# Optimization experiments

Measured on AMD Instinct MI355X. Metric: run time of the kernel, lower is better.

## Reference

```python
import jax, jax.numpy as jnp
import numpy as np

HID, NH, HD, MD = 512, 8, 64, 16  # hidden_dim, num_heads, head_dim, manifold_dim
B, S = 4, 1024
FLOW_STEPS, DT = 10, 0.1
EPS = 1e-8


def _cplx_weight(k, shape, std=0.02):
    kr, ki = jax.random.split(k)
    w = jax.random.normal(kr, shape) + 1j * jax.random.normal(ki, shape)
    return (w * std).astype(jnp.complex64)


def setup_inputs() -> dict:
    key = jax.random.key(0)
    ks = jax.random.split(key, 12)
    inp = {}
    inp['x_real'] = jax.random.normal(ks[0], (B, S, HID), dtype=jnp.float32)
    inp['x_imag'] = jax.random.normal(ks[1], (B, S, HID), dtype=jnp.float32)
    # manifold projection head_dim -> manifold_dim
    inp['Wm'] = _cplx_weight(ks[2], (MD, HD), std=HD ** -0.5)
    inp['bm'] = jnp.zeros((MD,), jnp.complex64)
    inp['Wq'] = _cplx_weight(ks[3], (MD, MD))
    inp['bq'] = jnp.zeros((MD,), jnp.complex64)
    inp['Wk'] = _cplx_weight(ks[4], (MD, MD))
    inp['bk'] = jnp.zeros((MD,), jnp.complex64)
    inp['Wv'] = _cplx_weight(ks[5], (MD, MD))
    inp['bv'] = jnp.zeros((MD,), jnp.complex64)
    # learned manifold metric (initialized to identity as in the module)
    inp['metric'] = jnp.eye(MD, dtype=jnp.complex64)
    # output projection expanded_dim = NH*MD -> hidden_dim
    inp['Wo'] = _cplx_weight(ks[6], (HID, NH * MD))
    inp['bo'] = jnp.zeros((HID,), jnp.complex64)
    return inp


def _forward(x_real, x_imag, Wm, bm, Wq, bq, Wk, bk, Wv, bv, metric, Wo, bo):
    x = (x_real + 1j * x_imag).astype(jnp.complex64)            # [B,S,HID]
    b, s, _ = x.shape
    h = x.reshape(b, s, NH, HD).transpose(0, 2, 1, 3)           # [B,NH,S,HD]
    # project onto low-dim manifold coordinates
    m = h @ Wm.T + bm                                           # [B,NH,S,MD]
    # hyperbolic exponential map at origin (curvature -1): tanh(|v|)/|v| * v
    n = jnp.sqrt(jnp.sum(jnp.abs(m) ** 2, -1, keepdims=True)) + EPS
    m = (jnp.tanh(n) / n) * m
    # parallel transport via the learned metric
    m = m @ metric
    # geometric flow: 10 Euler integration steps with dt=0.1
    sym = 0.5 * (metric + metric.conj().T)

    def step(carry, _):
        vel = carry @ sym - carry
        return carry + DT * vel, None

    m, _ = jax.lax.scan(step, m, None, length=FLOW_STEPS)
    # hyperbolic logarithm map at origin: artanh(|u|)/|u| * u
    n2 = jnp.sqrt(jnp.sum(jnp.abs(m) ** 2, -1, keepdims=True))
    n2 = jnp.clip(n2, EPS, 1.0 - 1e-6)
    m = (jnp.arctanh(n2) / n2) * m
    # complex q/k/v attention on manifold coordinates
    q = m @ Wq.T + bq
    k = m @ Wk.T + bk
    v = m @ Wv.T + bv
    scale = HD ** -0.5  # module uses self.scale = head_dim ** -0.5
    scores = jnp.einsum('bhsd,bhtd->bhst', q, jnp.conj(k)).real * scale  # [B,NH,S,S]
    attn = jax.nn.softmax(scores, axis=-1).astype(jnp.complex64)
    out = jnp.einsum('bhst,bhtd->bhsd', attn, v)                # [B,NH,S,MD]
    expanded = out.transpose(0, 2, 1, 3).reshape(b, s, NH * MD)  # [B,S,NH*MD]
    return expanded @ Wo.T + bo + x                              # residual, [B,S,HID]


def reference(x_real, x_imag, Wm, bm, Wq, bq, Wk, bk, Wv, bv, metric, Wo, bo):
    return _forward(x_real, x_imag, Wm, bm, Wq, bq, Wk, bk, Wv, bv, metric, Wo, bo)
```

## Files before the change

kernel.cpp:

```cpp
#include <hip/hip_runtime.h>
#include <math.h>

#define HIDD 512
#define NHH 8
#define HDD 64
#define MDD 16
#define Bz 4
#define Sz 1024
#define DTf 0.1f
#define EPSf 1e-8f
#define SCALEf 0.125f

typedef unsigned short ushort_t;
typedef unsigned int uint_t;

typedef __attribute__((ext_vector_type(8))) short bf16x8;
typedef __attribute__((ext_vector_type(4))) float f32x4;

constexpr size_t OFF_QB   = 0;
constexpr size_t OFF_KB   = OFF_QB + 262144;
constexpr size_t OFF_VT   = OFF_KB + 262144;
constexpr size_t OFF_E    = OFF_VT + 262144;
constexpr size_t OFF_T    = OFF_E + (size_t)Bz * Sz * NHH * MDD;
constexpr size_t OFF_WOT  = OFF_T + 256;
constexpr size_t OFF_FLAG = OFF_WOT + 512 * 128;

__device__ __forceinline__ float bf2f(ushort_t u) {
  union { unsigned int i; float f; } c;
  c.i = ((unsigned int)u) << 16;
  return c.f;
}
__device__ __forceinline__ ushort_t f2bf(float f) {
  unsigned int x = __float_as_uint(f);
  unsigned int r = (x + 0x7fffu + ((x >> 16) & 1u)) >> 16;
  return (ushort_t)r;
}
__device__ __forceinline__ float2 ldc(const void* p, int i, bool bf) {
  if (bf) {
    ushort2 u = ((const ushort2*)p)[i];
    return make_float2(bf2f(u.x), bf2f(u.y));
  }
  return ((const float2*)p)[i];
}
__device__ __forceinline__ float ldr(const void* p, size_t i, bool bf) {
  if (bf) return bf2f(((const ushort_t*)p)[i]);
  return ((const float*)p)[i];
}
__device__ __forceinline__ float2 cmadd(float2 acc, float2 a, float2 b) {
  acc.x = fmaf(a.x, b.x, fmaf(-a.y, b.y, acc.x));
  acc.y = fmaf(a.x, b.y, fmaf(a.y, b.x, acc.y));
  return acc;
}

__global__ __launch_bounds__(256) void k_setup(const void* __restrict__ metric,
                                               const ushort_t* __restrict__ xr_u,
                                               const void* __restrict__ Wo,
                                               int* __restrict__ flags,
                                               float2* __restrict__ Tg,
                                               float2* __restrict__ WoT) {
  __shared__ float2 mets[256], Ms[256], Ps2[256];
  __shared__ int votes[4];
  const uint_t* mu = (const uint_t*)metric;
  bool cbf = (mu[0] == 0x00003F80u);
  int tid = threadIdx.x;
  if (blockIdx.x == 0) {
    unsigned e = (xr_u[tid] >> 7) & 0xFFu;
    unsigned long long bal = __ballot(e >= 100u && e <= 134u);
    if ((tid & 63) == 0) votes[tid >> 6] = (int)__popcll(bal);
    __syncthreads();
    if (tid == 0) {
      int c = votes[0] + votes[1] + votes[2] + votes[3];
      flags[0] = cbf ? 1 : 0;
      flags[1] = (c > 192) ? 1 : 0;
    }
    int i = tid >> 4, j = tid & 15;
    mets[tid] = ldc(metric, tid, cbf);
    __syncthreads();
    float2 a = mets[tid];
    float2 bt = mets[j * 16 + i];
    float2 symv = make_float2(0.5f * (a.x + bt.x), 0.5f * (a.y - bt.y));
    float2 Mv = make_float2(DTf * symv.x, DTf * symv.y);
    if (i == j) Mv.x += 1.0f - DTf;
    Ms[tid] = Mv;
    Ps2[tid] = Mv;
    __syncthreads();
    for (int it = 0; it < 9; it++) {
      float2 acc = make_float2(0.f, 0.f);
      #pragma unroll
      for (int k = 0; k < 16; k++) acc = cmadd(acc, Ps2[i * 16 + k], Ms[k * 16 + j]);
      __syncthreads();
      Ps2[tid] = acc;
      __syncthreads();
    }
    float2 acc = make_float2(0.f, 0.f);
    #pragma unroll
    for (int k = 0; k < 16; k++) acc = cmadd(acc, mets[i * 16 + k], Ps2[k * 16 + j]);
    Tg[tid] = acc;
  } else {
    int idx = (blockIdx.x - 1) * 256 + tid;
    int o = idx >> 7, j = idx & 127;
    WoT[(size_t)j * 512 + o] = ldc(Wo, idx, cbf);
  }
}

__global__ __launch_bounds__(256) void k_qkv(
    const void* __restrict__ xr, const void* __restrict__ xi,
    const void* __restrict__ Wm, const void* __restrict__ bm,
    const void* __restrict__ Wq, const void* __restrict__ bq,
    const void* __restrict__ Wk, const void* __restrict__ bk,
    const void* __restrict__ Wv, const void* __restrict__ bv,
    const float2* __restrict__ Tg, const int* __restrict__ flags,
    ushort_t* __restrict__ Qb, ushort_t* __restrict__ Kb,
    ushort_t* __restrict__ VTb) {
  __shared__ float2 hs[64 * 65];
  __shared__ float2 msc[64 * 17];
  __shared__ float2 wmt[64 * 16];
  __shared__ float2 Tm[256];
  __shared__ float2 wqt[256], wkt[256], wvt[256];
  __shared__ float2 bms[16], bqs[16], bks[16], bvs[16];
  float2* msc2 = hs;

  bool cbf = flags[0] != 0;
  bool xbf = flags[1] != 0;
  int tid = threadIdx.x;
  int bh = blockIdx.y;
  int s0 = blockIdx.x * 64;

  size_t xoff = ((size_t)(((bh >> 3) * Sz) + s0)) * HIDD + (bh & 7) * HDD;
  if (xbf) {
    const ushort_t* xrb = (const ushort_t*)xr + xoff;
    const ushort_t* xib = (const ushort_t*)xi + xoff;
    #pragma unroll
    for (int it = 0; it < 4; it++) {
      int idx = tid + it * 256;
      int i = idx >> 4, e4 = idx & 15;
      ushort4 ur = ((const ushort4*)(xrb + (size_t)i * HIDD))[e4];
      ushort4 ui = ((const ushort4*)(xib + (size_t)i * HIDD))[e4];
      int e = e4 * 4;
      hs[i * 65 + e + 0] = make_float2(bf2f(ur.x), bf2f(ui.x));
      hs[i * 65 + e + 1] = make_float2(bf2f(ur.y), bf2f(ui.y));
      hs[i * 65 + e + 2] = make_float2(bf2f(ur.z), bf2f(ui.z));
      hs[i * 65 + e + 3] = make_float2(bf2f(ur.w), bf2f(ui.w));
    }
  } else {
    const float* xrb = (const float*)xr + xoff;
    const float* xib = (const float*)xi + xoff;
    #pragma unroll
    for (int it = 0; it < 4; it++) {
      int idx = tid + it * 256;
      int i = idx >> 4, e4 = idx & 15;
      float4 fr = ((const float4*)(xrb + (size_t)i * HIDD))[e4];
      float4 fi = ((const float4*)(xib + (size_t)i * HIDD))[e4];
      int e = e4 * 4;
      hs[i * 65 + e + 0] = make_float2(fr.x, fi.x);
      hs[i * 65 + e + 1] = make_float2(fr.y, fi.y);
      hs[i * 65 + e + 2] = make_float2(fr.z, fi.z);
      hs[i * 65 + e + 3] = make_float2(fr.w, fi.w);
    }
  }
  #pragma unroll
  for (int it = 0; it < 4; it++) {
    int c = tid + it * 256;
    int d = c >> 6, e = c & 63;
    wmt[e * 16 + d] = ldc(Wm, c, cbf);
  }
  {
    int j = tid >> 4, d = tid & 15;
    Tm[tid] = Tg[tid];
    wqt[d * 16 + j] = ldc(Wq, tid, cbf);
    wkt[d * 16 + j] = ldc(Wk, tid, cbf);
    wvt[d * 16 + j] = ldc(Wv, tid, cbf);
    if (tid < 16) {
      bms[tid] = ldc(bm, tid, cbf); bqs[tid] = ldc(bq, tid, cbf);
      bks[tid] = ldc(bk, tid, cbf); bvs[tid] = ldc(bv, tid, cbf);
    }
  }
  __syncthreads();

  int tok = tid >> 2, g = tid & 3;
  int jb = g * 4;

  float2 acc[4];
  #pragma unroll
  for (int i2 = 0; i2 < 4; i2++) acc[i2] = bms[jb + i2];
  for (int e = 0; e < 64; e++) {
    float2 hv = hs[tok * 65 + e];
    #pragma unroll
    for (int i2 = 0; i2 < 4; i2++) acc[i2] = cmadd(acc[i2], hv, wmt[e * 16 + jb + i2]);
  }
  float nn = 0.f;
  #pragma unroll
  for (int i2 = 0; i2 < 4; i2++) nn += acc[i2].x * acc[i2].x + acc[i2].y * acc[i2].y;
  nn += __shfl_xor(nn, 1);
  nn += __shfl_xor(nn, 2);
  float n1 = sqrtf(nn) + EPSf;
  float sc1 = tanhf(n1) / n1;
  #pragma unroll
  for (int i2 = 0; i2 < 4; i2++)
    msc[tok * 17 + jb + i2] = make_float2(acc[i2].x * sc1, acc[i2].y * sc1);
  __syncthreads();

  float2 m2[4];
  #pragma unroll
  for (int i2 = 0; i2 < 4; i2++) m2[i2] = make_float2(0.f, 0.f);
  for (int d = 0; d < 16; d++) {
    float2 mv = msc[tok * 17 + d];
    #pragma unroll
    for (int i2 = 0; i2 < 4; i2++) m2[i2] = cmadd(m2[i2], mv, Tm[d * 16 + jb + i2]);
  }
  float nn2 = 0.f;
  #pragma unroll
  for (int i2 = 0; i2 < 4; i2++) nn2 += m2[i2].x * m2[i2].x + m2[i2].y * m2[i2].y;
  nn2 += __shfl_xor(nn2, 1);
  nn2 += __shfl_xor(nn2, 2);
  float n2 = sqrtf(nn2);
  n2 = fminf(fmaxf(n2, EPSf), 1.0f - 1e-6f);
  float fac = atanhf(n2) / n2;
  #pragma unroll
  for (int i2 = 0; i2 < 4; i2++)
    msc2[tok * 17 + jb + i2] = make_float2(m2[i2].x * fac, m2[i2].y * fac);
  __syncthreads();

  float2 qa[4], ka[4], va[4];
  #pragma unroll
  for (int i2 = 0; i2 < 4; i2++) { qa[i2] = bqs[jb + i2]; ka[i2] = bks[jb + i2]; va[i2] = bvs[jb + i2]; }
  for (int d = 0; d < 16; d++) {
    float2 mv = msc2[tok * 17 + d];
    #pragma unroll
    for (int i2 = 0; i2 < 4; i2++) {
      qa[i2] = cmadd(qa[i2], mv, wqt[d * 16 + jb + i2]);
      ka[i2] = cmadd(ka[i2], mv, wkt[d * 16 + jb + i2]);
      va[i2] = cmadd(va[i2], mv, wvt[d * 16 + jb + i2]);
    }
  }
  int s = s0 + tok;
  uint_t qp[4], kp[4];
  #pragma unroll
  for (int i2 = 0; i2 < 4; i2++) {
    qp[i2] = (uint_t)f2bf(qa[i2].x * SCALEf) | ((uint_t)f2bf(qa[i2].y * SCALEf) << 16);
    kp[i2] = (uint_t)f2bf(ka[i2].x) | ((uint_t)f2bf(ka[i2].y) << 16);
  }
  size_t rowbase = ((size_t)bh * Sz + s) * 32 + (size_t)g * 8;
  *(uint4*)(Qb + rowbase) = make_uint4(qp[0], qp[1], qp[2], qp[3]);
  *(uint4*)(Kb + rowbase) = make_uint4(kp[0], kp[1], kp[2], kp[3]);
  size_t vtb = (size_t)bh * 32 * Sz;
  #pragma unroll
  for (int i2 = 0; i2 < 4; i2++) {
    int d = (jb + i2) * 2;
    VTb[vtb + (size_t)d * Sz + s]       = f2bf(va[i2].x);
    VTb[vtb + (size_t)(d + 1) * Sz + s] = f2bf(va[i2].y);
  }
}

__global__ __launch_bounds__(256) void k_attn_mf(const ushort_t* __restrict__ Qb,
                                                 const ushort_t* __restrict__ Kb,
                                                 const ushort_t* __restrict__ VTb,
                                                 float* __restrict__ ef) {
  __shared__ ushort_t Ks[128 * 88];
  __shared__ ushort_t VTs[32 * 152];
  __shared__ ushort_t Ps[4 * 16 * 40];
  int tid = threadIdx.x;
  int w = tid >> 6, lane = tid & 63;
  int n = lane & 15, qd = lane >> 4;
  int bh = blockIdx.y;
  int qb = blockIdx.x * 64 + w * 16;

  const ushort_t* Qh = Qb + (size_t)bh * Sz * 32;
  const ushort_t* Kh = Kb + (size_t)bh * Sz * 32;
  const ushort_t* VTh = VTb + (size_t)bh * 32 * Sz;

  bf16x8 qf = *(const bf16x8*)(Qh + (size_t)(qb + n) * 32 + qd * 8);

  f32x4 o0 = {0.f, 0.f, 0.f, 0.f}, o1 = {0.f, 0.f, 0.f, 0.f};
  float m_run = -INFINITY, l_run = 0.f;
  ushort_t* Pw = Ps + w * 16 * 40;

  for (int kc = 0; kc < Sz; kc += 128) {
    __syncthreads();
    {
      int row = tid >> 1, half = tid & 1;
      const uint4* sk = (const uint4*)(Kh + (size_t)(kc + row) * 32 + half * 16);
      uint4 a = sk[0], b2 = sk[1];
      *(uint4*)(Ks + row * 88 + half * 16) = a;
      *(uint4*)(Ks + row * 88 + half * 16 + 8) = b2;
      int d = tid >> 3, seg = tid & 7;
      const uint4* sv = (const uint4*)(VTh + (size_t)d * Sz + kc + seg * 16);
      uint4 c = sv[0], e2 = sv[1];
      *(uint4*)(VTs + d * 152 + seg * 16) = c;
      *(uint4*)(VTs + d * 152 + seg * 16 + 8) = e2;
    }
    __syncthreads();
    #pragma unroll
    for (int st = 0; st < 4; st++) {
      int kb = st * 32;
      bf16x8 ka0 = *(const bf16x8*)(Ks + (kb + n) * 88 + qd * 8);
      bf16x8 ka1 = *(const bf16x8*)(Ks + (kb + 16 + n) * 88 + qd * 8);
      f32x4 z = {0.f, 0.f, 0.f, 0.f};
      f32x4 st0 = __builtin_amdgcn_mfma_f32_16x16x32_bf16(ka0, qf, z, 0, 0, 0);
      f32x4 st1 = __builtin_amdgcn_mfma_f32_16x16x32_bf16(ka1, qf, z, 0, 0, 0);
      float mt = fmaxf(fmaxf(fmaxf(st0[0], st0[1]), fmaxf(st0[2], st0[3])),
                       fmaxf(fmaxf(st1[0], st1[1]), fmaxf(st1[2], st1[3])));
      mt = fmaxf(mt, __shfl_xor(mt, 16));
      mt = fmaxf(mt, __shfl_xor(mt, 32));
      float mnew = fmaxf(m_run, mt);
      float alpha = __expf(m_run - mnew);
      float p0[4], p1[4];
      #pragma unroll
      for (int r = 0; r < 4; r++) {
        p0[r] = __expf(st0[r] - mnew);
        p1[r] = __expf(st1[r] - mnew);
      }
      float ls = (p0[0] + p0[1]) + (p0[2] + p0[3])
               + (p1[0] + p1[1]) + (p1[2] + p1[3]);
      ls += __shfl_xor(ls, 16);
      ls += __shfl_xor(ls, 32);
      l_run = fmaf(l_run, alpha, ls);
      m_run = mnew;
      #pragma unroll
      for (int r = 0; r < 4; r++) {
        Pw[n * 40 + qd * 4 + r]      = f2bf(p0[r]);
        Pw[n * 40 + 16 + qd * 4 + r] = f2bf(p1[r]);
      }
      bf16x8 pa = *(const bf16x8*)(Pw + n * 40 + qd * 8);
      bf16x8 vb0 = *(const bf16x8*)(VTs + n * 152 + kb + qd * 8);
      bf16x8 vb1 = *(const bf16x8*)(VTs + (n + 16) * 152 + kb + qd * 8);
      float ar0 = __shfl(alpha, qd * 4 + 0);
      float ar1 = __shfl(alpha, qd * 4 + 1);
      float ar2 = __shfl(alpha, qd * 4 + 2);
      float ar3 = __shfl(alpha, qd * 4 + 3);
      f32x4 oo0, oo1;
      oo0[0] = o0[0] * ar0; oo0[1] = o0[1] * ar1; oo0[2] = o0[2] * ar2; oo0[3] = o0[3] * ar3;
      oo1[0] = o1[0] * ar0; oo1[1] = o1[1] * ar1; oo1[2] = o1[2] * ar2; oo1[3] = o1[3] * ar3;
      o0 = __builtin_amdgcn_mfma_f32_16x16x32_bf16(pa, vb0, oo0, 0, 0, 0);
      o1 = __builtin_amdgcn_mfma_f32_16x16x32_bf16(pa, vb1, oo1, 0, 0, 0);
    }
  }
  int b = bh >> 3, h = bh & 7;
  #pragma unroll
  for (int r = 0; r < 4; r++) {
    float li = __shfl(l_run, qd * 4 + r);
    float inv = 1.0f / li;
    int tok = qb + qd * 4 + r;
    float* ep = ef + (((size_t)(b * Sz + tok)) * NHH + h) * 32;
    ep[n]      = o0[r] * inv;
    ep[16 + n] = o1[r] * inv;
  }
}

__global__ __launch_bounds__(256) void k_proj_r(const float2* __restrict__ ew,
                                                const float2* __restrict__ WoT,
                                                const void* __restrict__ bo,
                                                const void* __restrict__ xr,
                                                const int* __restrict__ flags,
                                                float* __restrict__ out) {
  __shared__ float2 es[8 * 128];
  bool cbf = flags[0] != 0;
  bool xbf = flags[1] != 0;
  int tid = threadIdx.x;
  int tok0 = (blockIdx.x >> 1) * 8;
  int o = (blockIdx.x & 1) * 256 + tid;
  #pragma unroll
  for (int it = 0; it < 4; it++) {
    int idx = tid + it * 256;
    es[idx] = ew[(size_t)tok0 * 128 + idx];
  }
  __syncthreads();
  float acc[8];
  #pragma unroll
  for (int t = 0; t < 8; t++) acc[t] = 0.f;
  #pragma unroll 8
  for (int j = 0; j < 128; j++) {
    float2 w = WoT[(size_t)j * 512 + o];
    #pragma unroll
    for (int t = 0; t < 8; t++) {
      float2 e = es[t * 128 + j];
      acc[t] = fmaf(e.x, w.x, fmaf(-e.y, w.y, acc[t]));
    }
  }
  float bor = ldc(bo, o, cbf).x;
  #pragma unroll
  for (int t = 0; t < 8; t++) {
    size_t gt = tok0 + t;
    out[gt * HIDD + o] = acc[t] + bor + ldr(xr, gt * HIDD + o, xbf);
  }
}

__global__ __launch_bounds__(256) void k_proj_c(const float2* __restrict__ ew,
                                                const float2* __restrict__ WoT,
                                                const void* __restrict__ bo,
                                                const void* __restrict__ xr,
                                                const void* __restrict__ xi,
                                                const int* __restrict__ flags,
                                                ushort2* __restrict__ out) {
  __shared__ float2 es[8 * 128];
  bool cbf = flags[0] != 0;
  bool xbf = flags[1] != 0;
  int tid = threadIdx.x;
  int tok0 = blockIdx.x * 8;
  #pragma unroll
  for (int it = 0; it < 4; it++) {
    int idx = tid + it * 256;
    es[idx] = ew[(size_t)tok0 * 128 + idx];
  }
  __syncthreads();
  for (int rep = 0; rep < 2; rep++) {
    int o = tid + rep * 256;
    float2 accT[8];
    #pragma unroll
    for (int t = 0; t < 8; t++) accT[t] = make_float2(0.f, 0.f);
    #pragma unroll 2
    for (int j = 0; j < 128; j++) {
      float2 wv = WoT[(size_t)j * 512 + o];
      #pragma unroll
      for (int t = 0; t < 8; t++) accT[t] = cmadd(accT[t], es[t * 128 + j], wv);
    }
    float2 bov = ldc(bo, o, cbf);
    #pragma unroll
    for (int t = 0; t < 8; t++) {
      size_t gt = tok0 + t;
      float rx = accT[t].x + bov.x + ldr(xr, gt * HIDD + o, xbf);
      float ry = accT[t].y + bov.y + ldr(xi, gt * HIDD + o, xbf);
      out[gt * HIDD + o] = make_ushort2(f2bf(ry), f2bf(rx));
    }
  }
}

extern "C" void kernel_launch(void* const* d_in, const int* in_sizes, int n_in,
                              void* d_out, int out_size, void* d_ws, size_t ws_size,
                              hipStream_t stream) {
  const void* xr     = d_in[0];
  const void* xi     = d_in[1];
  const void* Wm     = d_in[2];
  const void* bm     = d_in[3];
  const void* Wq     = d_in[4];
  const void* bq     = d_in[5];
  const void* Wk     = d_in[6];
  const void* bk     = d_in[7];
  const void* Wv     = d_in[8];
  const void* bv     = d_in[9];
  const void* metric = d_in[10];
  const void* Wo     = d_in[11];
  const void* bo     = d_in[12];

  float2* W = (float2*)d_ws;
  int* flags = (int*)(W + OFF_FLAG);
  ushort_t* Qb  = (ushort_t*)(W + OFF_QB);
  ushort_t* Kb  = (ushort_t*)(W + OFF_KB);
  ushort_t* VTb = (ushort_t*)(W + OFF_VT);

  k_setup<<<257, 256, 0, stream>>>(metric, (const ushort_t*)xr, Wo, flags,
                                   W + OFF_T, W + OFF_WOT);
  k_qkv<<<dim3(16, 32), 256, 0, stream>>>(xr, xi, Wm, bm, Wq, bq, Wk, bk, Wv, bv,
                                          W + OFF_T, flags, Qb, Kb, VTb);
  k_attn_mf<<<dim3(16, 32), 256, 0, stream>>>(Qb, Kb, VTb, (float*)(W + OFF_E));
  if (out_size == Bz * Sz * HIDD) {
    k_proj_r<<<1024, 256, 0, stream>>>(W + OFF_E, W + OFF_WOT, bo, xr, flags,
                                       (float*)d_out);
  } else {
    k_proj_c<<<512, 256, 0, stream>>>(W + OFF_E, W + OFF_WOT, bo, xr, xi, flags,
                                      (ushort2*)d_out);
  }
}
```

Before: 161.0 us.

## Drop setup kernel, fold metric power and Wo transpose into later kernels

Removes the separate setup launch. Each block of the qkv kernel now recomputes the metric flow-power matrix itself, each projection kernel re-derives the dtype flags locally, and the Wo transpose moves into the attention kernel. The attention inner loop is restructured to compute all eight score tiles for a 128-key chunk at once, with one max reduction per chunk, lazy rescaling when the max grows by more than 8, per-lane partial row sums, and s_setprio around the MFMAs. tanh and atanh are replaced by fast exp/log forms. The risks are redundant per-block work for the matrix power and reduced accuracy from the lazy max and the fast math.

Result: faster. 149.3 us (-7.2%).

```diff
diff --git a/kernel.cpp b/kernel.cpp
--- a/kernel.cpp
+++ b/kernel.cpp
@@ -21,9 +21,7 @@
 constexpr size_t OFF_KB   = OFF_QB + 262144;
 constexpr size_t OFF_VT   = OFF_KB + 262144;
 constexpr size_t OFF_E    = OFF_VT + 262144;
-constexpr size_t OFF_T    = OFF_E + (size_t)Bz * Sz * NHH * MDD;
-constexpr size_t OFF_WOT  = OFF_T + 256;
-constexpr size_t OFF_FLAG = OFF_WOT + 512 * 128;
+constexpr size_t OFF_WOT  = OFF_E + (size_t)Bz * Sz * NHH * MDD;
 
 __device__ __forceinline__ float bf2f(ushort_t u) {
   union { unsigned int i; float f; } c;
@@ -50,57 +48,6 @@
   acc.x = fmaf(a.x, b.x, fmaf(-a.y, b.y, acc.x));
   acc.y = fmaf(a.x, b.y, fmaf(a.y, b.x, acc.y));
   return acc;
-}
-
-__global__ __launch_bounds__(256) void k_setup(const void* __restrict__ metric,
-                                               const ushort_t* __restrict__ xr_u,
-                                               const void* __restrict__ Wo,
-                                               int* __restrict__ flags,
-                                               float2* __restrict__ Tg,
-                                               float2* __restrict__ WoT) {
-  __shared__ float2 mets[256], Ms[256], Ps2[256];
-  __shared__ int votes[4];
-  const uint_t* mu = (const uint_t*)metric;
-  bool cbf = (mu[0] == 0x00003F80u);
-  int tid = threadIdx.x;
-  if (blockIdx.x == 0) {
-    unsigned e = (xr_u[tid] >> 7) & 0xFFu;
-    unsigned long long bal = __ballot(e >= 100u && e <= 134u);
-    if ((tid & 63) == 0) votes[tid >> 6] = (int)__popcll(bal);
-    __syncthreads();
-    if (tid == 0) {
-      int c = votes[0] + votes[1] + votes[2] + votes[3];
-      flags[0] = cbf ? 1 : 0;
-      flags[1] = (c > 192) ? 1 : 0;
-    }
-    int i = tid >> 4, j = tid & 15;
-    mets[tid] = ldc(metric, tid, cbf);
-    __syncthreads();
-    float2 a = mets[tid];
-    float2 bt = mets[j * 16 + i];
-    float2 symv = make_float2(0.5f * (a.x + bt.x), 0.5f * (a.y - bt.y));
-    float2 Mv = make_float2(DTf * symv.x, DTf * symv.y);
-    if (i == j) Mv.x += 1.0f - DTf;
-    Ms[tid] = Mv;
-    Ps2[tid] = Mv;
-    __syncthreads();
-    for (int it = 0; it < 9; it++) {
-      float2 acc = make_float2(0.f, 0.f);
-      #pragma unroll
-      for (int k = 0; k < 16; k++) acc = cmadd(acc, Ps2[i * 16 + k], Ms[k * 16 + j]);
-      __syncthreads();
-      Ps2[tid] = acc;
-      __syncthreads();
-    }
-    float2 acc = make_float2(0.f, 0.f);
-    #pragma unroll
-    for (int k = 0; k < 16; k++) acc = cmadd(acc, mets[i * 16 + k], Ps2[k * 16 + j]);
-    Tg[tid] = acc;
-  } else {
-    int idx = (blockIdx.x - 1) * 256 + tid;
-    int o = idx >> 7, j = idx & 127;
-    WoT[(size_t)j * 512 + o] = ldc(Wo, idx, cbf);
-  }
 }
 
 __global__ __launch_bounds__(256) void k_qkv(
@@ -109,7 +56,7 @@
     const void* __restrict__ Wq, const void* __restrict__ bq,
     const void* __restrict__ Wk, const void* __restrict__ bk,
     const void* __restrict__ Wv, const void* __restrict__ bv,
-    const float2* __restrict__ Tg, const int* __restrict__ flags,
+    const void* __restrict__ metric,
     ushort_t* __restrict__ Qb, ushort_t* __restrict__ Kb,
     ushort_t* __restrict__ VTb) {
   __shared__ float2 hs[64 * 65];
@@ -118,13 +65,49 @@
   __shared__ float2 Tm[256];
   __shared__ float2 wqt[256], wkt[256], wvt[256];
   __shared__ float2 bms[16], bqs[16], bks[16], bvs[16];
+  __shared__ int votes[4];
   float2* msc2 = hs;
 
-  bool cbf = flags[0] != 0;
-  bool xbf = flags[1] != 0;
   int tid = threadIdx.x;
   int bh = blockIdx.y;
   int s0 = blockIdx.x * 64;
+
+  const uint_t* mu = (const uint_t*)metric;
+  bool cbf = (mu[0] == 0x00003F80u);
+
+  {
+    unsigned e = (((const ushort_t*)xr)[tid] >> 7) & 0xFFu;
+    unsigned long long bal = __ballot(e >= 100u && e <= 134u);
+    if ((tid & 63) == 0) votes[tid >> 6] = (int)__popcll(bal);
+  }
+
+  {
+    int i = tid >> 4, j = tid & 15;
+    wqt[tid] = ldc(metric, tid, cbf);
+    __syncthreads();
+    float2 a = wqt[tid];
+    float2 bt = wqt[j * 16 + i];
+    float2 symv = make_float2(0.5f * (a.x + bt.x), 0.5f * (a.y - bt.y));
+    float2 Mv = make_float2(DTf * symv.x, DTf * symv.y);
+    if (i == j) Mv.x += 1.0f - DTf;
+    wkt[tid] = Mv;
+    wvt[tid] = Mv;
+    __syncthreads();
+    for (int it = 0; it < 9; it++) {
+      float2 acc = make_float2(0.f, 0.f);
+      #pragma unroll
+      for (int k = 0; k < 16; k++) acc = cmadd(acc, wvt[i * 16 + k], wkt[k * 16 + j]);
+      __syncthreads();
+      wvt[tid] = acc;
+      __syncthreads();
+    }
+    float2 acc = make_float2(0.f, 0.f);
+    #pragma unroll
+    for (int k = 0; k < 16; k++) acc = cmadd(acc, wqt[i * 16 + k], wvt[k * 16 + j]);
+    Tm[tid] = acc;
+    __syncthreads();
+  }
+  bool xbf = (votes[0] + votes[1] + votes[2] + votes[3]) > 192;
 
   size_t xoff = ((size_t)(((bh >> 3) * Sz) + s0)) * HIDD + (bh & 7) * HDD;
   if (xbf) {
@@ -166,7 +149,6 @@
   }
   {
     int j = tid >> 4, d = tid & 15;
-    Tm[tid] = Tg[tid];
     wqt[d * 16 + j] = ldc(Wq, tid, cbf);
     wkt[d * 16 + j] = ldc(Wk, tid, cbf);
     wvt[d * 16 + j] = ldc(Wv, tid, cbf);
@@ -194,7 +176,8 @@
   nn += __shfl_xor(nn, 1);
   nn += __shfl_xor(nn, 2);
   float n1 = sqrtf(nn) + EPSf;
-  float sc1 = tanhf(n1) / n1;
+  float te = __expf(2.f * n1);
+  float sc1 = (te - 1.f) / ((te + 1.f) * n1);
   #pragma unroll
   for (int i2 = 0; i2 < 4; i2++)
     msc[tok * 17 + jb + i2] = make_float2(acc[i2].x * sc1, acc[i2].y * sc1);
@@ -215,7 +198,7 @@
   nn2 += __shfl_xor(nn2, 2);
   float n2 = sqrtf(nn2);
   n2 = fminf(fmaxf(n2, EPSf), 1.0f - 1e-6f);
-  float fac = atanhf(n2) / n2;
+  float fac = 0.5f * __logf((1.f + n2) / (1.f - n2)) / n2;
   #pragma unroll
   for (int i2 = 0; i2 < 4; i2++)
     msc2[tok * 17 + jb + i2] = make_float2(m2[i2].x * fac, m2[i2].y * fac);
@@ -255,11 +238,24 @@
 __global__ __launch_bounds__(256) void k_attn_mf(const ushort_t* __restrict__ Qb,
                                                  const ushort_t* __restrict__ Kb,
                                                  const ushort_t* __restrict__ VTb,
-                                                 float* __restrict__ ef) {
+                                                 float* __restrict__ ef,
+                                                 const void* __restrict__ Wo,
+                                                 float2* __restrict__ WoT,
+                                                 const void* __restrict__ metric) {
   __shared__ ushort_t Ks[128 * 88];
   __shared__ ushort_t VTs[32 * 152];
-  __shared__ ushort_t Ps[4 * 16 * 40];
+  __shared__ ushort_t Ps[4 * 16 * 136];
   int tid = threadIdx.x;
+
+  {
+    bool cbf = (((const uint_t*)metric)[0] == 0x00003F80u);
+    if (tid < 128) {
+      int idx = (blockIdx.y * 16 + blockIdx.x) * 128 + tid;
+      int o = idx >> 7, j = idx & 127;
+      WoT[(size_t)j * 512 + o] = ldc(Wo, idx, cbf);
+    }
+  }
+
   int w = tid >> 6, lane = tid & 63;
   int n = lane & 15, qd = lane >> 4;
   int bh = blockIdx.y;
@@ -272,8 +268,8 @@
   bf16x8 qf = *(const bf16x8*)(Qh + (size_t)(qb + n) * 32 + qd * 8);
 
   f32x4 o0 = {0.f, 0.f, 0.f, 0.f}, o1 = {0.f, 0.f, 0.f, 0.f};
-  float m_run = -INFINITY, l_run = 0.f;
-  ushort_t* Pw = Ps + w * 16 * 40;
+  float m_run = 0.f, l_run = 0.f;
+  ushort_t* Pw = Ps + w * 16 * 136;
 
   for (int kc = 0; kc < Sz; kc += 128) {
     __syncthreads();
@@ -290,51 +286,74 @@
       *(uint4*)(VTs + d * 152 + seg * 16 + 8) = e2;
     }
     __syncthreads();
-    #pragma unroll
-    for (int st = 0; st < 4; st++) {
-      int kb = st * 32;
-      bf16x8 ka0 = *(const bf16x8*)(Ks + (kb + n) * 88 + qd * 8);
-      bf16x8 ka1 = *(const bf16x8*)(Ks + (kb + 16 + n) * 88 + qd * 8);
+
+    f32x4 st[8];
+    __builtin_amdgcn_s_setprio(1);
+    #pragma unroll
+    for (int s = 0; s < 4; s++) {
+      bf16x8 ka0 = *(const bf16x8*)(Ks + (s * 32 + n) * 88 + qd * 8);
+      bf16x8 ka1 = *(const bf16x8*)(Ks + (s * 32 + 16 + n) * 88 + qd * 8);
       f32x4 z = {0.f, 0.f, 0.f, 0.f};
-      f32x4 st0 = __builtin_amdgcn_mfma_f32_16x16x32_bf16(ka0, qf, z, 0, 0, 0);
-      f32x4 st1 = __builtin_amdgcn_mfma_f32_16x16x32_bf16(ka1, qf, z, 0, 0, 0);
-      float mt = fmaxf(fmaxf(fmaxf(st0[0], st0[1]), fmaxf(st0[2], st0[3])),
-                       fmaxf(fmaxf(st1[0], st1[1]), fmaxf(st1[2], st1[3])));
-      mt = fmaxf(mt, __shfl_xor(mt, 16));
-      mt = fmaxf(mt, __shfl_xor(mt, 32));
+      st[2 * s]     = __builtin_amdgcn_mfma_f32_16x16x32_bf16(ka0, qf, z, 0, 0, 0);
+      st[2 * s + 1] = __builtin_amdgcn_mfma_f32_16x16x32_bf16(ka1, qf, z, 0, 0, 0);
+    }
+    __builtin_amdgcn_s_setprio(0);
+
+    float mt = st[0][0];
+    #pragma unroll
+    for (int i = 0; i < 8; i++) {
+      #pragma unroll
+      for (int r = 0; r < 4; r++) mt = fmaxf(mt, st[i][r]);
+    }
+    mt = fmaxf(mt, __shfl_xor(mt, 16));
+    mt = fmaxf(mt, __shfl_xor(mt, 32));
+    if (!__all(mt - m_run <= 8.f)) {
       float mnew = fmaxf(m_run, mt);
       float alpha = __expf(m_run - mnew);
-      float p0[4], p1[4];
-      #pragma unroll
-      for (int r = 0; r < 4; r++) {
-        p0[r] = __expf(st0[r] - mnew);
-        p1[r] = __expf(st1[r] - mnew);
-      }
-      float ls = (p0[0] + p0[1]) + (p0[2] + p0[3])
-               + (p1[0] + p1[1]) + (p1[2] + p1[3]);
-      ls += __shfl_xor(ls, 16);
-      ls += __shfl_xor(ls, 32);
-      l_run = fmaf(l_run, alpha, ls);
-      m_run = mnew;
-      #pragma unroll
-      for (int r = 0; r < 4; r++) {
-        Pw[n * 40 + qd * 4 + r]      = f2bf(p0[r]);
-        Pw[n * 40 + 16 + qd * 4 + r] = f2bf(p1[r]);
-      }
-      bf16x8 pa = *(const bf16x8*)(Pw + n * 40 + qd * 8);
-      bf16x8 vb0 = *(const bf16x8*)(VTs + n * 152 + kb + qd * 8);
-      bf16x8 vb1 = *(const bf16x8*)(VTs + (n + 16) * 152 + kb + qd * 8);
+      l_run *= alpha;
       float ar0 = __shfl(alpha, qd * 4 + 0);
       float ar1 = __shfl(alpha, qd * 4 + 1);
       float ar2 = __shfl(alpha, qd * 4 + 2);
       float ar3 = __shfl(alpha, qd * 4 + 3);
-      f32x4 oo0, oo1;
-      oo0[0] = o0[0] * ar0; oo0[1] = o0[1] * ar1; oo0[2] = o0[2] * ar2; oo0[3] = o0[3] * ar3;
-      oo1[0] = o1[0] * ar0; oo1[1] = o1[1] * ar1; oo1[2] = o1[2] * ar2; oo1[3] = o1[3] * ar3;
-      o0 = __builtin_amdgcn_mfma_f32_16x16x32_bf16(pa, vb0, oo0, 0, 0, 0);
-      o1 = __builtin_amdgcn_mfma_f32_16x16x32_bf16(pa, vb1, oo1, 0, 0, 0);
-    }
-  }
+      o0[0] *= ar0; o0[1] *= ar1; o0[2] *= ar2; o0[3] *= ar3;
+      o1[0] *= ar0; o1[1] *= ar1; o1[2] *= ar2; o1[3] *= ar3;
+      m_run = mnew;
+    }
+
+    float lt = 0.f;
+    #pragma unroll
+    for (int s = 0; s < 4; s++) {
+      float p0[4], p1[4];
+      #pragma unroll
+      for (int r = 0; r < 4; r++) {
+        p0[r] = __expf(st[2 * s][r] - m_run);
+        p1[r] = __expf(st[2 * s + 1][r] - m_run);
+        lt += p0[r] + p1[r];
+      }
+      uint2 w0, w1;
+      w0.x = (uint_t)f2bf(p0[0]) | ((uint_t)f2bf(p0[1]) << 16);
+      w0.y = (uint_t)f2bf(p0[2]) | ((uint_t)f2bf(p0[3]) << 16);
+      w1.x = (uint_t)f2bf(p1[0]) | ((uint_t)f2bf(p1[1]) << 16);
+      w1.y = (uint_t)f2bf(p1[2]) | ((uint_t)f2bf(p1[3]) << 16);
+      *(uint2*)(Pw + n * 136 + s * 32 + qd * 4) = w0;
+      *(uint2*)(Pw + n * 136 + s * 32 + 16 + qd * 4) = w1;
+    }
+    l_run += lt;
+
+    __builtin_amdgcn_s_setprio(1);
+    #pragma unroll
+    for (int s = 0; s < 4; s++) {
+      bf16x8 pa  = *(const bf16x8*)(Pw + n * 136 + s * 32 + qd * 8);
+      bf16x8 vb0 = *(const bf16x8*)(VTs + n * 152 + s * 32 + qd * 8);
+      bf16x8 vb1 = *(const bf16x8*)(VTs + (n + 16) * 152 + s * 32 + qd * 8);
+      o0 = __builtin_amdgcn_mfma_f32_16x16x32_bf16(pa, vb0, o0, 0, 0, 0);
+      o1 = __builtin_amdgcn_mfma_f32_16x16x32_bf16(pa, vb1, o1, 0, 0, 0);
+    }
+    __builtin_amdgcn_s_setprio(0);
+  }
+
+  l_run += __shfl_xor(l_run, 16);
+  l_run += __shfl_xor(l_run, 32);
   int b = bh >> 3, h = bh & 7;
   #pragma unroll
   for (int r = 0; r < 4; r++) {
@@ -351,12 +370,17 @@
                                                 const float2* __restrict__ WoT,
                                                 const void* __restrict__ bo,
                                                 const void* __restrict__ xr,
-                                                const int* __restrict__ flags,
+                                                const void* __restrict__ metric,
                                                 float* __restrict__ out) {
   __shared__ float2 es[8 * 128];
-  bool cbf = flags[0] != 0;
-  bool xbf = flags[1] != 0;
+  __shared__ int votes[4];
   int tid = threadIdx.x;
+  bool cbf = (((const uint_t*)metric)[0] == 0x00003F80u);
+  {
+    unsigned e = (((const ushort_t*)xr)[tid] >> 7) & 0xFFu;
+    unsigned long long bal = __ballot(e >= 100u && e <= 134u);
+    if ((tid & 63) == 0) votes[tid >> 6] = (int)__popcll(bal);
+  }
   int tok0 = (blockIdx.x >> 1) * 8;
   int o = (blockIdx.x & 1) * 256 + tid;
   #pragma unroll
@@ -365,6 +389,7 @@
     es[idx] = ew[(size_t)tok0 * 128 + idx];
   }
   __syncthreads();
+  bool xbf = (votes[0] + votes[1] + votes[2] + votes[3]) > 192;
   float acc[8];
   #pragma unroll
   for (int t = 0; t < 8; t++) acc[t] = 0.f;
@@ -390,12 +415,17 @@
                                                 const void* __restrict__ bo,
                                                 const void* __restrict__ xr,
                                                 const void* __restrict__ xi,
-                                                const int* __restrict__ flags,
+                                                const void* __restrict__ metric,
                                                 ushort2* __restrict__ out) {
   __shared__ float2 es[8 * 128];
-  bool cbf = flags[0] != 0;
-  bool xbf = flags[1] != 0;
+  __shared__ int votes[4];
   int tid = threadIdx.x;
+  bool cbf = (((const uint_t*)metric)[0] == 0x00003F80u);
+  {
+    unsigned e = (((const ushort_t*)xr)[tid] >> 7) & 0xFFu;
+    unsigned long long bal = __ballot(e >= 100u && e <= 134u);
+    if ((tid & 63) == 0) votes[tid >> 6] = (int)__popcll(bal);
+  }
   int tok0 = blockIdx.x * 8;
   #pragma unroll
   for (int it = 0; it < 4; it++) {
@@ -403,6 +433,7 @@
     es[idx] = ew[(size_t)tok0 * 128 + idx];
   }
   __syncthreads();
+  bool xbf = (votes[0] + votes[1] + votes[2] + votes[3]) > 192;
   for (int rep = 0; rep < 2; rep++) {
     int o = tid + rep * 256;
     float2 accT[8];
@@ -443,21 +474,19 @@
   const void* bo     = d_in[12];
 
   float2* W = (float2*)d_ws;
-  int* flags = (int*)(W + OFF_FLAG);
   ushort_t* Qb  = (ushort_t*)(W + OFF_QB);
   ushort_t* Kb  = (ushort_t*)(W + OFF_KB);
   ushort_t* VTb = (ushort_t*)(W + OFF_VT);
 
-  k_setup<<<257, 256, 0, stream>>>(metric, (const ushort_t*)xr, Wo, flags,
-                                   W + OFF_T, W + OFF_WOT);
   k_qkv<<<dim3(16, 32), 256, 0, stream>>>(xr, xi, Wm, bm, Wq, bq, Wk, bk, Wv, bv,
-                                          W + OFF_T, flags, Qb, Kb, VTb);
-  k_attn_mf<<<dim3(16, 32), 256, 0, stream>>>(Qb, Kb, VTb, (float*)(W + OFF_E));
+                                          metric, Qb, Kb, VTb);
+  k_attn_mf<<<dim3(16, 32), 256, 0, stream>>>(Qb, Kb, VTb, (float*)(W + OFF_E),
+                                              Wo, W + OFF_WOT, metric);
   if (out_size == Bz * Sz * HIDD) {
-    k_proj_r<<<1024, 256, 0, stream>>>(W + OFF_E, W + OFF_WOT, bo, xr, flags,
+    k_proj_r<<<1024, 256, 0, stream>>>(W + OFF_E, W + OFF_WOT, bo, xr, metric,
                                        (float*)d_out);
   } else {
-    k_proj_c<<<512, 256, 0, stream>>>(W + OFF_E, W + OFF_WOT, bo, xr, xi, flags,
+    k_proj_c<<<512, 256, 0, stream>>>(W + OFF_E, W + OFF_WOT, bo, xr, xi, metric,
                                       (ushort2*)d_out);
   }
 }
```
